# Kernel optimization log

Measured on AMD Instinct MI355X. Metric: run time of the kernel, lower is better.

Reference implementation:

```python
import jax, jax.numpy as jnp
import numpy as np

# hyperparameters (see init_kwargs)
DP, DS, DO, D, K, C = 256, 256, 64, 320, 10, 10
SI, NS = 100, 22
ALIGN = 0.05
COEF = 0.3989422917366028  # 1/sqrt(2*pi)
B, SEQ, T_STEPS = 32, 512, 200


def _linear_params(key, fan_in, fan_out):
    # torch nn.Linear default init: U(-1/sqrt(fan_in), 1/sqrt(fan_in))
    s = 1.0 / np.sqrt(fan_in)
    kw, kb = jax.random.split(key)
    w = jax.random.uniform(kw, (fan_in, fan_out), minval=-s, maxval=s, dtype=jnp.float32)
    b = jax.random.uniform(kb, (fan_out,), minval=-s, maxval=s, dtype=jnp.float32)
    return w, b


def setup_inputs() -> dict:
    key = jax.random.key(0)
    ks = jax.random.split(key, 8)
    sentence = jax.random.randint(ks[0], (B, SEQ), 0, SI)
    speaker_id = jax.random.randint(ks[1], (B,), 0, NS)
    Lut_P = jax.random.normal(ks[2], (SI, DP), dtype=jnp.float32)
    Lut_S = jax.random.normal(ks[3], (NS, DS), dtype=jnp.float32)
    Na_w, Na_b = _linear_params(ks[4], D * K, 3 * C)
    Nu_w, Nu_b = _linear_params(ks[5], D * K, D)
    No_w, No_b = _linear_params(ks[6], D * K, DO)
    kf = jax.random.split(ks[7], 2)
    Fu_w, Fu_b = _linear_params(kf[0], DS, DP)
    Fo_w, Fo_b = _linear_params(kf[1], DS, D * K)
    return dict(sentence=sentence, speaker_id=speaker_id, Lut_P=Lut_P, Lut_S=Lut_S,
                Na_w=Na_w, Na_b=Na_b, Nu_w=Nu_w, Nu_b=Nu_b, No_w=No_w, No_b=No_b,
                Fu_w=Fu_w, Fu_b=Fu_b, Fo_w=Fo_w, Fo_b=Fo_b, T=T_STEPS)


def reference(sentence, speaker_id, Lut_P, Lut_S, Na_w, Na_b, Nu_w, Nu_b,
              No_w, No_b, Fu_w, Fu_b, Fo_w, Fo_b, T):
    batch, seq_len = sentence.shape
    # Encoder: embedding lookups
    lut_p = Lut_P[sentence]          # (B, S, dp)
    ident = Lut_S[speaker_id]        # (B, ds)

    # ident-dependent terms are loop-invariant; hoist out of the scan
    idt = jnp.tanh(ident @ Fu_w + Fu_b)   # (B, dp)
    fo = ident @ Fo_w + Fo_b              # (B, d*k)

    # initialize(): buffer seeded with speaker embedding in first dp rows
    S0 = jnp.zeros((batch, D, K), dtype=lut_p.dtype)
    S0 = S0.at[:, :DP, :].set(ident[:, :, None])
    mu0 = jnp.zeros((batch, C), dtype=lut_p.dtype)
    o0 = jnp.zeros((batch, DO), dtype=lut_p.dtype)

    J = jnp.arange(1, seq_len + 1, dtype=lut_p.dtype)  # (S,)

    def step(carry, _):
        S_tm1, mu_tm1, o_tm1 = carry
        # --- GMM attention ---
        out = (S_tm1.reshape(batch, D * K) @ Na_w + Na_b).reshape(batch, 3, C)
        k_t, b_t, y_t = out[:, 0], out[:, 1], out[:, 2]
        mu_t = mu_tm1 + ALIGN * jnp.exp(k_t)            # (B, c)
        sig_t = jnp.exp(b_t)                            # (B, c)
        g_t = jax.nn.softmax(y_t, axis=1)               # (B, c)
        # phi: (B, c, S)
        phi = g_t[:, :, None] * jnp.exp(-0.5 * sig_t[:, :, None] * (mu_t[:, :, None] - J) ** 2)
        alpha = COEF * phi.sum(axis=1)                  # (B, S)
        c_t = jnp.einsum('bs,bsd->bd', alpha, lut_p)    # (B, dp)
        # --- Decoder buffer update ---
        C_t = jnp.concatenate([c_t + idt, o_tm1 / 30.0], axis=1)        # (B, d)
        Sp = jnp.concatenate([C_t[:, :, None], S_tm1[:, :, :-1]], axis=2)  # (B, d, k)
        u = Sp.reshape(batch, D * K) @ Nu_w + Nu_b                      # (B, d)
        S_t = jnp.concatenate([u[:, :, None], S_tm1[:, :, :-1]], axis=2)
        o_t = (S_t.reshape(batch, D * K) + fo) @ No_w + No_b            # (B, do)
        return (S_t, mu_t, o_t), o_t

    (_, _, _), outs = jax.lax.scan(step, (S0, mu0, o0), None, length=T)
    return outs  # (T, B, do)
```

## Files before the change

kernel.cpp:

```cpp
#include <hip/hip_runtime.h>

#define DP   256
#define DD   320
#define KK   10
#define CC   10
#define DOUT 64
#define SEQn 512
#define BB   32
#define SI   100
#define NSL  32
#define NGR  8
#define BPG  4
#define NTH  640
#define DPS  10
#define RPS  100

#define CFBASE 1024
#define PSA   448
#define UF_O  0
#define ZA_O  40
#define ZO_O  168
#define HALF_A (NGR*NSL*PSA)
#define PSB   320
#define PUBA_OFF 2048
#define PUBB_OFF (PUBA_OFF + 2*HALF_A)

typedef float f4 __attribute__((ext_vector_type(4)));

__device__ __forceinline__ void llc_ld(f4* dst, const float* p) {
    f4 r;
    asm volatile("global_load_dwordx4 %0, %1, off sc0 sc1" : "=&v"(r) : "v"(p));
    asm volatile("s_waitcnt vmcnt(0)" ::: "memory");
    __builtin_amdgcn_sched_barrier(0);
    *dst = r;
}
__device__ __forceinline__ void llc_st(float* p, f4 v) {
    asm volatile("global_store_dwordx4 %0, %1, off sc0 sc1" :: "v"(p), "v"(v) : "memory");
}

__global__ void prep_kernel(int* ctr) {
    int i = blockIdx.x * blockDim.x + threadIdx.x;
    if (i < 2048) ctr[i] = 0;
}

__device__ __forceinline__ void gbar8(int* base, int slice, int target) {
    asm volatile("s_waitcnt vmcnt(0)" ::: "memory");
    __syncthreads();
    if (threadIdx.x == 0)
        __hip_atomic_fetch_add(&base[(slice & 7) * 16], 1, __ATOMIC_RELEASE, __HIP_MEMORY_SCOPE_AGENT);
    if (threadIdx.x < 8) {
        for (;;) {
            int v = __hip_atomic_load(&base[threadIdx.x * 16], __ATOMIC_RELAXED, __HIP_MEMORY_SCOPE_AGENT);
            v += __shfl_xor(v, 1, 8);
            v += __shfl_xor(v, 2, 8);
            v += __shfl_xor(v, 4, 8);
            if (v >= target) break;
            __builtin_amdgcn_s_sleep(2);
        }
    }
    __syncthreads();
}

__global__ __launch_bounds__(NTH) void recur_kernel(
    const int* __restrict__ sentence, const int* __restrict__ speaker,
    const float* __restrict__ LutP, const float* __restrict__ LutS,
    const float* __restrict__ NaW,  const float* __restrict__ NaB,
    const float* __restrict__ NuW,  const float* __restrict__ NuB,
    const float* __restrict__ NoW,  const float* __restrict__ NoB,
    const float* __restrict__ FuW,  const float* __restrict__ FuB,
    const float* __restrict__ FoW,  const float* __restrict__ FoB,
    float* __restrict__ ws, const int* __restrict__ Tptr,
    float* __restrict__ out)
{
    const int tid  = threadIdx.x;
    const int s    = blockIdx.x & (NSL - 1);
    const int g    = blockIdx.x >> 5;
    const bool owner = (s < BPG);
    const int dbase = s * DPS;
    const int rbase = s * RPS;
    int*  ctr  = (int*)ws + g * 128;
    int*  CFg  = (int*)ws + CFBASE + g * 64;
    float* pubA = ws + PUBA_OFF;
    float* pubB = ws + PUBB_OFF;

    const int c_   = tid >> 6;
    const int lane = tid & 63;

    __shared__ float xsE[BPG][3328];
    __shared__ float wNa[RPS][32];
    __shared__ float wNo[RPS][65];
    __shared__ float naT0[DPS][32];
    __shared__ float noT0[DPS][65];
    __shared__ float identsh[BPG][DP];
    __shared__ float ufull[BPG][DD];
    __shared__ float colL[BPG][DD];
    __shared__ float ucol[BPG*DPS];
    __shared__ float zr[BPG*32];
    __shared__ float zor[BPG*DOUT];
    __shared__ float zastage[NSL][32];
    __shared__ float zostage[NSL][DOUT];
    __shared__ float fos[BPG][RPS];
    __shared__ float nubO[DPS];
    __shared__ float nabL[32];
    __shared__ float aoutL[32];
    __shared__ float muL[CC], sgL[CC], ggL[CC];
    __shared__ float alphaL[SEQn];
    __shared__ float histL[SI];
    __shared__ float idtF[DP];
    __shared__ float colF[DD];
    __shared__ float o_own[DOUT];
    __shared__ float foNoL[DOUT];
    __shared__ int   sentL[SEQn];
    __shared__ int   posidx[SEQn];
    __shared__ int   vstart[SI + 1];
    __shared__ int   vcnt[SI];

    for (int i = tid; i < RPS * 30; i += NTH) {
        int r = i / 30, c = i % 30;
        wNa[r][c] = NaW[(rbase + r) * 30 + c];
    }
    for (int i = tid; i < RPS * 64; i += NTH) {
        int r = i / 64, o = i % 64;
        wNo[r][o] = NoW[(rbase + r) * 64 + o];
    }
    if (tid < DPS * 30) { int dl = tid / 30, c = tid % 30; naT0[dl][c] = NaW[((dbase + dl) * KK) * 30 + c]; }
    if (tid < DPS * 64) { int dl = tid >> 6, o = tid & 63; noT0[dl][o] = NoW[((dbase + dl) * KK) * 64 + o]; }
    if (tid < DPS) nubO[tid] = NuB[dbase + tid];
    if (tid >= 16 && tid < 48) { int c = tid - 16; nabL[c] = (c < 30) ? NaB[c] : 0.f; }
    for (int i = tid; i < BPG * DP; i += NTH) {
        int j = i / DP, v = i % DP;
        identsh[j][v] = LutS[speaker[g * BPG + j] * DP + v];
    }
    __syncthreads();

    float w[50];
    #pragma unroll
    for (int q = 0; q < 50; ++q)
        w[q] = NuW[(size_t)(lane * 50 + q) * DD + dbase + c_];

    for (int i = tid; i < BPG * RPS; i += NTH) {
        int j = i / RPS, r = i % RPS;
        float acc = FoB[rbase + r];
        for (int v = 0; v < DP; v += 8) {
            float wv[8];
            #pragma unroll
            for (int e = 0; e < 8; ++e) wv[e] = FoW[(v + e) * 3200 + rbase + r];
            #pragma unroll
            for (int e = 0; e < 8; ++e) acc += identsh[j][v + e] * wv[e];
        }
        fos[j][r] = acc;
    }
    if (owner) {
        if (tid < DP) {
            float acc = FuB[tid];
            for (int v = 0; v < DP; v += 8) {
                float wv[8];
                #pragma unroll
                for (int e = 0; e < 8; ++e) wv[e] = FuW[(v + e) * DP + tid];
                #pragma unroll
                for (int e = 0; e < 8; ++e) acc += identsh[s][v + e] * wv[e];
            }
            idtF[tid] = tanhf(acc);
        }
        if (tid >= 512 && tid < 512 + CC) muL[tid - 512] = 0.f;
        if (tid < SEQn) sentL[tid] = sentence[(g * BPG + s) * SEQn + tid];
        __syncthreads();
        if (tid < SI) { int cnt = 0; for (int q = 0; q < SEQn; ++q) if (sentL[q] == tid) ++cnt; vcnt[tid] = cnt; }
        __syncthreads();
        if (tid == 0) { int run = 0; for (int v = 0; v < SI; ++v) { vstart[v] = run; run += vcnt[v]; } vstart[SI] = run; }
        __syncthreads();
        if (tid < SI) { int k = vstart[tid]; for (int q = 0; q < SEQn; ++q) if (sentL[q] == tid) posidx[k++] = q; }
    }
    for (int i = tid; i < BPG * 3200; i += NTH) {
        int j = i / 3200, row = i % 3200;
        int d = row / KK;
        xsE[j][(row / 50) * 52 + (row % 50)] = (d < DP) ? identsh[j][d] : 0.f;
    }
    __syncthreads();
    if (tid < 128) {
        int j = tid >> 5, c = tid & 31;
        float acc = 0.f;
        if (c < 30)
            for (int rr = 0; rr < RPS; ++rr) {
                int row = rbase + rr;
                acc += xsE[j][(row / 50) * 52 + (row % 50)] * wNa[rr][c];
            }
        zr[j * 32 + c] = acc;
    }
    if (tid >= 128 && tid < 384) {
        int t = tid - 128, j = t >> 6, o = t & 63;
        float acc = 0.f;
        for (int rr = 0; rr < RPS; ++rr) acc += fos[j][rr] * wNo[rr][o];
        zor[j * 64 + o] = acc;
    }
    __syncthreads();
    {
        float* pa0 = pubA + (size_t)(g * NSL + s) * PSA;
        if (tid < 32) llc_st(pa0 + ZA_O + tid * 4, *(f4*)&zr[tid * 4]);
        if (tid >= 32 && tid < 96) { int q = tid - 32; llc_st(pa0 + ZO_O + q * 4, *(f4*)&zor[q * 4]); }
    }
    gbar8(ctr, s, 32 * 1);

    const int T = Tptr[0];

    for (int i = 0; i < T; ++i) {
        const int rh = i & 1, wh = rh ^ 1;
        float* pa_r = pubA + (size_t)rh * HALF_A + (size_t)g * NSL * PSA;
        float* pa_w = pubA + (size_t)wh * HALF_A + (size_t)(g * NSL + s) * PSA;

        if (i > 0 && tid < 320) {
            int p = tid / 10, q = tid % 10;
            f4 v; llc_ld(&v, pa_r + p * PSA + UF_O + q * 4);
            #pragma unroll
            for (int e = 0; e < 4; ++e) {
                int f = q * 4 + e;
                ufull[f / 10][p * 10 + (f % 10)] = v[e];
            }
        }
        __syncthreads();

        if (owner) {
            f4 v_za = {0.f,0.f,0.f,0.f}, v_zo = {0.f,0.f,0.f,0.f};
            if (tid < 256) {
                const float* p = pa_r + (tid >> 3) * PSA + ZA_O + s * 32 + (tid & 7) * 4;
                asm volatile("global_load_dwordx4 %0, %1, off sc0 sc1" : "=&v"(v_za) : "v"(p));
            }
            if (tid < 512) {
                const float* p = pa_r + (tid >> 4) * PSA + ZO_O + s * 64 + (tid & 15) * 4;
                asm volatile("global_load_dwordx4 %0, %1, off sc0 sc1" : "=&v"(v_zo) : "v"(p));
            }
            asm volatile("s_waitcnt vmcnt(0)" ::: "memory");
            __builtin_amdgcn_sched_barrier(0);
            if (tid < 256) *(f4*)&zastage[tid >> 3][(tid & 7) * 4] = v_za;
            if (tid < 512) *(f4*)&zostage[tid >> 4][(tid & 15) * 4] = v_zo;
            __syncthreads();
            if (tid < 30) {
                float a = nabL[tid];
                for (int p = 0; p < NSL; ++p) a += zastage[p][tid];
                aoutL[tid] = a;
            }
            if (tid >= 64 && tid < 128) {
                int o = tid - 64;
                float v = 0.f;
                for (int p = 0; p < NSL; ++p) v += zostage[p][o];
                if (i == 0) { foNoL[o] = NoB[o] + v; o_own[o] = 0.f; }
                else        o_own[o] = foNoL[o] + v;
            }
            __syncthreads();
            if (tid < CC) {
                muL[tid] += 0.05f * expf(aoutL[tid]);
                sgL[tid] = expf(aoutL[10 + tid]);
                float m = -1e30f;
                for (int q = 0; q < CC; ++q) m = fmaxf(m, aoutL[20 + q]);
                float ssum = 0.f;
                for (int q = 0; q < CC; ++q) ssum += expf(aoutL[20 + q] - m);
                ggL[tid] = expf(aoutL[20 + tid] - m) / ssum;
            }
            __syncthreads();
            if (tid < SEQn) {
                float J = (float)(tid + 1);
                float a = 0.f;
                #pragma unroll
                for (int c = 0; c < CC; ++c) { float dm = muL[c] - J; a += ggL[c] * __expf(-0.5f * sgL[c] * dm * dm); }
                alphaL[tid] = a * 0.3989422917366028f;
            }
            __syncthreads();
            if (tid < SI) {
                float h = 0.f;
                for (int k = vstart[tid]; k < vstart[tid + 1]; ++k) h += alphaL[posidx[k]];
                histL[tid] = h;
            }
            __syncthreads();
            if (tid < DP) {
                float acc = idtF[tid];
                for (int v = 0; v < SI; v += 10) {
                    float wv[10];
                    #pragma unroll
                    for (int e = 0; e < 10; ++e) wv[e] = LutP[(v + e) * DP + tid];
                    #pragma unroll
                    for (int e = 0; e < 10; ++e) acc += histL[v + e] * wv[e];
                }
                colF[tid] = acc;
            } else if (tid < DD) {
                colF[tid] = o_own[tid - DP] * (1.0f / 30.0f);
            }
            __syncthreads();
            if (i > 0 && tid < DOUT)
                out[((size_t)(i - 1) * BB + (g * BPG + s)) * DOUT + tid] = o_own[tid];
            if (tid < 80) llc_st(pubB + (size_t)(g * BPG + s) * PSB + tid * 4, *(f4*)&colF[tid * 4]);
            asm volatile("s_waitcnt vmcnt(0)" ::: "memory");
            __syncthreads();
            if (tid == 0)
                __hip_atomic_store(&CFg[s * 16], i + 1, __ATOMIC_RELEASE, __HIP_MEMORY_SCOPE_AGENT);
        }

        for (int it = tid; it < BPG * DD; it += NTH) {
            int j = it / DD, d = it % DD;
            float* p = &xsE[j][(d / 5) * 52 + (d % 5) * 10];
            float t0 = p[0];
            float v1 = p[1], v2 = p[2], v3 = p[3], v4 = p[4], v5 = p[5], v6 = p[6], v7 = p[7], v8 = p[8];
            p[1] = (i == 0) ? t0 : ufull[j][d];
            p[2] = v1; p[3] = v2; p[4] = v3; p[5] = v4; p[6] = v5; p[7] = v6; p[8] = v7; p[9] = v8;
        }
        if (tid < BPG) {
            while (__hip_atomic_load(&CFg[tid * 16], __ATOMIC_RELAXED, __HIP_MEMORY_SCOPE_AGENT) < i + 1)
                __builtin_amdgcn_s_sleep(2);
        }
        __syncthreads();

        if (tid < 320) {
            int j = tid / 80, q = tid % 80;
            f4 v; llc_ld(&v, pubB + (size_t)(g * BPG + j) * PSB + q * 4);
            #pragma unroll
            for (int e = 0; e < 4; ++e) colL[j][q * 4 + e] = v[e];
        }
        __syncthreads();
        for (int it = tid; it < BPG * DD; it += NTH) {
            int j = it / DD, d = it % DD;
            xsE[j][(d / 5) * 52 + (d % 5) * 10] = colL[j][d];
        }
        __syncthreads();

        {
            float accE[BPG];
            #pragma unroll
            for (int j = 0; j < BPG; ++j) {
                const float* xb = &xsE[j][lane * 52];
                float a = 0.f;
                #pragma unroll
                for (int qq = 0; qq < 12; ++qq) {
                    f4 x = *(const f4*)(xb + qq * 4);
                    a += x.x * w[qq * 4] + x.y * w[qq * 4 + 1] + x.z * w[qq * 4 + 2] + x.w * w[qq * 4 + 3];
                }
                a += xb[48] * w[48] + xb[49] * w[49];
                accE[j] = a;
            }
            #pragma unroll
            for (int j = 0; j < BPG; ++j)
                for (int off = 32; off; off >>= 1) accE[j] += __shfl_xor(accE[j], off, 64);
            if (lane == 0) {
                #pragma unroll
                for (int j = 0; j < BPG; ++j) ucol[j * DPS + c_] = accE[j] + nubO[c_];
            }
        }
        __syncthreads();

        if (tid < 128) {
            int j = tid >> 5, c = tid & 31;
            float acc = 0.f;
            if (c < 30) {
                for (int dd = 0; dd < DPS; ++dd) {
                    int rg = 2 * s + (dd >= 5);
                    int of = dd * 10 - (dd >= 5 ? 50 : 0);
                    const float* xb = &xsE[j][rg * 52 + of];
                    #pragma unroll
                    for (int k = 1; k < KK; ++k) acc += xb[k] * wNa[dd * 10 + k][c];
                }
                #pragma unroll
                for (int dl = 0; dl < DPS; ++dl) acc += ucol[j * DPS + dl] * naT0[dl][c];
            }
            zr[j * 32 + c] = acc;
        }
        if (tid >= 128 && tid < 384) {
            int t = tid - 128, j = t >> 6, o = t & 63;
            float acc = 0.f;
            for (int dd = 0; dd < DPS; ++dd) {
                int rg = 2 * s + (dd >= 5);
                int of = dd * 10 - (dd >= 5 ? 50 : 0);
                const float* xb = &xsE[j][rg * 52 + of];
                #pragma unroll
                for (int k = 1; k < KK; ++k) acc += xb[k] * wNo[dd * 10 + k][o];
            }
            #pragma unroll
            for (int dl = 0; dl < DPS; ++dl) acc += ucol[j * DPS + dl] * noT0[dl][o];
            zor[j * 64 + o] = acc;
        }
        __syncthreads();

        if (tid < 10)                llc_st(pa_w + UF_O + tid * 4,        *(f4*)&ucol[tid * 4]);
        if (tid >= 10 && tid < 42)  { int q = tid - 10; llc_st(pa_w + ZA_O + q * 4, *(f4*)&zr[q * 4]); }
        if (tid >= 42 && tid < 106) { int q = tid - 42; llc_st(pa_w + ZO_O + q * 4, *(f4*)&zor[q * 4]); }
        gbar8(ctr, s, 32 * (i + 2));
    }

    if (owner) {
        const float* pa_r = pubA + (size_t)(T & 1) * HALF_A + (size_t)g * NSL * PSA;
        if (tid < 512) {
            f4 v; llc_ld(&v, pa_r + (tid >> 4) * PSA + ZO_O + s * 64 + (tid & 15) * 4);
            *(f4*)&zostage[tid >> 4][(tid & 15) * 4] = v;
        }
        __syncthreads();
        if (tid < DOUT) {
            float v = foNoL[tid];
            for (int p = 0; p < NSL; ++p) v += zostage[p][tid];
            out[((size_t)(T - 1) * BB + (g * BPG + s)) * DOUT + tid] = v;
        }
    }
}

extern "C" void kernel_launch(void* const* d_in, const int* in_sizes, int n_in,
                              void* d_out, int out_size, void* d_ws, size_t ws_size,
                              hipStream_t stream) {
    const int*   sentence = (const int*)d_in[0];
    const int*   speaker  = (const int*)d_in[1];
    const float* LutP = (const float*)d_in[2];
    const float* LutS = (const float*)d_in[3];
    const float* NaW  = (const float*)d_in[4];
    const float* NaB  = (const float*)d_in[5];
    const float* NuW  = (const float*)d_in[6];
    const float* NuB  = (const float*)d_in[7];
    const float* NoW  = (const float*)d_in[8];
    const float* NoB  = (const float*)d_in[9];
    const float* FuW  = (const float*)d_in[10];
    const float* FuB  = (const float*)d_in[11];
    const float* FoW  = (const float*)d_in[12];
    const float* FoB  = (const float*)d_in[13];
    const int*   Tptr = (const int*)d_in[14];
    float* ws   = (float*)d_ws;
    float* outp = (float*)d_out;

    hipLaunchKernelGGL(prep_kernel, dim3(2), dim3(1024), 0, stream, (int*)d_ws);
    hipLaunchKernelGGL(recur_kernel, dim3(NSL * NGR), dim3(NTH), 0, stream,
                       sentence, speaker, LutP, LutS, NaW, NaB,
                       NuW, NuB, NoW, NoB, FuW, FuB, FoW, FoB,
                       ws, Tptr, outp);
}
```

Baseline: 4.701 ms.

## Compute attention redundantly in every block to drop owner-to-slice handoff

Every block in a group now computes the attention, histogram and context column for all four batch rows itself, where before the four owner blocks did this and published the result through a separate buffer with a per-step flag spin-wait. This removes one cross-block synchronisation and a global round-trip per step. The partial sums are also stored transposed (slice-major per output element), so each reader reduces 32 contiguous values with wide loads instead of staging and summing in shared memory. The cost is four times the attention work in every block, serialised over the batch rows, plus more shared memory and scalar stores.

```diff
diff --git a/kernel.cpp b/kernel.cpp
--- a/kernel.cpp
+++ b/kernel.cpp
@@ -15,15 +15,9 @@
 #define DPS  10
 #define RPS  100
 
-#define CFBASE 1024
-#define PSA   448
-#define UF_O  0
-#define ZA_O  40
-#define ZO_O  168
-#define HALF_A (NGR*NSL*PSA)
-#define PSB   320
+#define GSZ   13568
+#define HALF  (NGR*GSZ)
 #define PUBA_OFF 2048
-#define PUBB_OFF (PUBA_OFF + 2*HALF_A)
 
 typedef float f4 __attribute__((ext_vector_type(4)));
 
@@ -36,6 +30,9 @@
 }
 __device__ __forceinline__ void llc_st(float* p, f4 v) {
     asm volatile("global_store_dwordx4 %0, %1, off sc0 sc1" :: "v"(p), "v"(v) : "memory");
+}
+__device__ __forceinline__ void llc_st1(float* p, float v) {
+    asm volatile("global_store_dword %0, %1, off sc0 sc1" :: "v"(p), "v"(v) : "memory");
 }
 
 __global__ void prep_kernel(int* ctr) {
@@ -75,13 +72,10 @@
     const int tid  = threadIdx.x;
     const int s    = blockIdx.x & (NSL - 1);
     const int g    = blockIdx.x >> 5;
-    const bool owner = (s < BPG);
     const int dbase = s * DPS;
     const int rbase = s * RPS;
     int*  ctr  = (int*)ws + g * 128;
-    int*  CFg  = (int*)ws + CFBASE + g * 64;
     float* pubA = ws + PUBA_OFF;
-    float* pubB = ws + PUBB_OFF;
 
     const int c_   = tid >> 6;
     const int lane = tid & 63;
@@ -91,29 +85,27 @@
     __shared__ float wNo[RPS][65];
     __shared__ float naT0[DPS][32];
     __shared__ float noT0[DPS][65];
-    __shared__ float identsh[BPG][DP];
     __shared__ float ufull[BPG][DD];
     __shared__ float colL[BPG][DD];
     __shared__ float ucol[BPG*DPS];
     __shared__ float zr[BPG*32];
     __shared__ float zor[BPG*DOUT];
-    __shared__ float zastage[NSL][32];
-    __shared__ float zostage[NSL][DOUT];
+    __shared__ float aout4[BPG][32];
+    __shared__ float oprev4[BPG][DOUT];
+    __shared__ float foNo4[BPG][DOUT];
+    __shared__ float mu4[BPG][CC], sg4[BPG][CC], gg4[BPG][CC];
+    __shared__ float alphaL[SEQn];
+    __shared__ float hist4[BPG][104];
+    __shared__ float idtF4[BPG][DP];
+    __shared__ float identsh[BPG][DP];
     __shared__ float fos[BPG][RPS];
     __shared__ float nubO[DPS];
     __shared__ float nabL[32];
-    __shared__ float aoutL[32];
-    __shared__ float muL[CC], sgL[CC], ggL[CC];
-    __shared__ float alphaL[SEQn];
-    __shared__ float histL[SI];
-    __shared__ float idtF[DP];
-    __shared__ float colF[DD];
-    __shared__ float o_own[DOUT];
-    __shared__ float foNoL[DOUT];
-    __shared__ int   sentL[SEQn];
-    __shared__ int   posidx[SEQn];
-    __shared__ int   vstart[SI + 1];
-    __shared__ int   vcnt[SI];
+    __shared__ float zred[DOUT][9];
+    __shared__ int   sentL4[BPG][SEQn];
+    __shared__ short posidx4[BPG][SEQn];
+    __shared__ int   vstart4[BPG][104];
+    __shared__ int   vcnt[104];
 
     for (int i = tid; i < RPS * 30; i += NTH) {
         int r = i / 30, c = i % 30;
@@ -127,10 +119,13 @@
     if (tid < DPS * 64) { int dl = tid >> 6, o = tid & 63; noT0[dl][o] = NoW[((dbase + dl) * KK) * 64 + o]; }
     if (tid < DPS) nubO[tid] = NuB[dbase + tid];
     if (tid >= 16 && tid < 48) { int c = tid - 16; nabL[c] = (c < 30) ? NaB[c] : 0.f; }
+    if (tid >= 64 && tid < 104) mu4[(tid - 64) / 10][(tid - 64) % 10] = 0.f;
     for (int i = tid; i < BPG * DP; i += NTH) {
         int j = i / DP, v = i % DP;
         identsh[j][v] = LutS[speaker[g * BPG + j] * DP + v];
     }
+    for (int i = tid; i < BPG * SEQn; i += NTH)
+        sentL4[i / SEQn][i % SEQn] = sentence[(g * BPG + i / SEQn) * SEQn + i % SEQn];
     __syncthreads();
 
     float w[50];
@@ -150,26 +145,26 @@
         }
         fos[j][r] = acc;
     }
-    if (owner) {
-        if (tid < DP) {
-            float acc = FuB[tid];
-            for (int v = 0; v < DP; v += 8) {
-                float wv[8];
-                #pragma unroll
-                for (int e = 0; e < 8; ++e) wv[e] = FuW[(v + e) * DP + tid];
-                #pragma unroll
-                for (int e = 0; e < 8; ++e) acc += identsh[s][v + e] * wv[e];
-            }
-            idtF[tid] = tanhf(acc);
-        }
-        if (tid >= 512 && tid < 512 + CC) muL[tid - 512] = 0.f;
-        if (tid < SEQn) sentL[tid] = sentence[(g * BPG + s) * SEQn + tid];
-        __syncthreads();
-        if (tid < SI) { int cnt = 0; for (int q = 0; q < SEQn; ++q) if (sentL[q] == tid) ++cnt; vcnt[tid] = cnt; }
-        __syncthreads();
-        if (tid == 0) { int run = 0; for (int v = 0; v < SI; ++v) { vstart[v] = run; run += vcnt[v]; } vstart[SI] = run; }
-        __syncthreads();
-        if (tid < SI) { int k = vstart[tid]; for (int q = 0; q < SEQn; ++q) if (sentL[q] == tid) posidx[k++] = q; }
+    for (int idx = tid; idx < BPG * DP; idx += NTH) {
+        int j = idx / DP, d = idx % DP;
+        float acc = FuB[d];
+        for (int v = 0; v < DP; v += 8) {
+            float wv[8];
+            #pragma unroll
+            for (int e = 0; e < 8; ++e) wv[e] = FuW[(v + e) * DP + d];
+            #pragma unroll
+            for (int e = 0; e < 8; ++e) acc += identsh[j][v + e] * wv[e];
+        }
+        idtF4[j][d] = tanhf(acc);
+    }
+    __syncthreads();
+    for (int j = 0; j < BPG; ++j) {
+        if (tid < SI) { int cnt = 0; for (int q = 0; q < SEQn; ++q) cnt += (sentL4[j][q] == tid); vcnt[tid] = cnt; }
+        __syncthreads();
+        if (tid == 0) { int run = 0; for (int v = 0; v < SI; ++v) { vstart4[j][v] = run; run += vcnt[v]; } vstart4[j][SI] = run; }
+        __syncthreads();
+        if (tid < SI) { int k = vstart4[j][tid]; for (int q = 0; q < SEQn; ++q) if (sentL4[j][q] == tid) posidx4[j][k++] = (short)q; }
+        __syncthreads();
     }
     for (int i = tid; i < BPG * 3200; i += NTH) {
         int j = i / 3200, row = i % 3200;
@@ -195,9 +190,9 @@
     }
     __syncthreads();
     {
-        float* pa0 = pubA + (size_t)(g * NSL + s) * PSA;
-        if (tid < 32) llc_st(pa0 + ZA_O + tid * 4, *(f4*)&zr[tid * 4]);
-        if (tid >= 32 && tid < 96) { int q = tid - 32; llc_st(pa0 + ZO_O + q * 4, *(f4*)&zor[q * 4]); }
+        float* pz = pubA + (size_t)g * GSZ + 1280;
+        if (tid < 128) { int j = tid >> 5, c = tid & 31; if (c < 30) llc_st1(pz + ((j * 96 + c) << 5) + s, zr[j * 32 + c]); }
+        if (tid >= 128 && tid < 384) { int t = tid - 128; int j = t >> 6, o = t & 63; llc_st1(pz + ((j * 96 + 32 + o) << 5) + s, zor[j * 64 + o]); }
     }
     gbar8(ctr, s, 32 * 1);
 
@@ -205,119 +200,127 @@
 
     for (int i = 0; i < T; ++i) {
         const int rh = i & 1, wh = rh ^ 1;
-        float* pa_r = pubA + (size_t)rh * HALF_A + (size_t)g * NSL * PSA;
-        float* pa_w = pubA + (size_t)wh * HALF_A + (size_t)(g * NSL + s) * PSA;
-
-        if (i > 0 && tid < 320) {
-            int p = tid / 10, q = tid % 10;
-            f4 v; llc_ld(&v, pa_r + p * PSA + UF_O + q * 4);
-            #pragma unroll
-            for (int e = 0; e < 4; ++e) {
-                int f = q * 4 + e;
-                ufull[f / 10][p * 10 + (f % 10)] = v[e];
-            }
-        }
-        __syncthreads();
-
-        if (owner) {
-            f4 v_za = {0.f,0.f,0.f,0.f}, v_zo = {0.f,0.f,0.f,0.f};
-            if (tid < 256) {
-                const float* p = pa_r + (tid >> 3) * PSA + ZA_O + s * 32 + (tid & 7) * 4;
-                asm volatile("global_load_dwordx4 %0, %1, off sc0 sc1" : "=&v"(v_za) : "v"(p));
-            }
-            if (tid < 512) {
-                const float* p = pa_r + (tid >> 4) * PSA + ZO_O + s * 64 + (tid & 15) * 4;
-                asm volatile("global_load_dwordx4 %0, %1, off sc0 sc1" : "=&v"(v_zo) : "v"(p));
+        const float* pa_r = pubA + (size_t)rh * HALF + (size_t)g * GSZ;
+        float* pa_w = pubA + (size_t)wh * HALF + (size_t)g * GSZ;
+
+        {
+            f4 zv0,zv1,zv2,zv3,zv4,zv5,zv6,zv7;
+            f4 ufa = {0,0,0,0}, ufb = {0,0,0,0};
+            const bool hz = (tid < 384);
+            const int zj = tid / 96, zc = tid % 96;
+            if (hz) {
+                const float* base = pa_r + 1280 + ((zj * 96 + zc) << 5);
+                asm volatile("global_load_dwordx4 %0, %1, off sc0 sc1" : "=&v"(zv0) : "v"(base));
+                asm volatile("global_load_dwordx4 %0, %1, off sc0 sc1" : "=&v"(zv1) : "v"(base + 4));
+                asm volatile("global_load_dwordx4 %0, %1, off sc0 sc1" : "=&v"(zv2) : "v"(base + 8));
+                asm volatile("global_load_dwordx4 %0, %1, off sc0 sc1" : "=&v"(zv3) : "v"(base + 12));
+                asm volatile("global_load_dwordx4 %0, %1, off sc0 sc1" : "=&v"(zv4) : "v"(base + 16));
+                asm volatile("global_load_dwordx4 %0, %1, off sc0 sc1" : "=&v"(zv5) : "v"(base + 20));
+                asm volatile("global_load_dwordx4 %0, %1, off sc0 sc1" : "=&v"(zv6) : "v"(base + 24));
+                asm volatile("global_load_dwordx4 %0, %1, off sc0 sc1" : "=&v"(zv7) : "v"(base + 28));
+            }
+            const bool hu = (i > 0 && tid >= 384);
+            const int ui = tid - 384;
+            if (hu) {
+                asm volatile("global_load_dwordx4 %0, %1, off sc0 sc1" : "=&v"(ufa) : "v"(pa_r + ui * 4));
+                if (ui < 64)
+                    asm volatile("global_load_dwordx4 %0, %1, off sc0 sc1" : "=&v"(ufb) : "v"(pa_r + (ui + 256) * 4));
             }
             asm volatile("s_waitcnt vmcnt(0)" ::: "memory");
             __builtin_amdgcn_sched_barrier(0);
-            if (tid < 256) *(f4*)&zastage[tid >> 3][(tid & 7) * 4] = v_za;
-            if (tid < 512) *(f4*)&zostage[tid >> 4][(tid & 15) * 4] = v_zo;
-            __syncthreads();
-            if (tid < 30) {
-                float a = nabL[tid];
-                for (int p = 0; p < NSL; ++p) a += zastage[p][tid];
-                aoutL[tid] = a;
-            }
-            if (tid >= 64 && tid < 128) {
-                int o = tid - 64;
+            if (hz) {
                 float v = 0.f;
-                for (int p = 0; p < NSL; ++p) v += zostage[p][o];
-                if (i == 0) { foNoL[o] = NoB[o] + v; o_own[o] = 0.f; }
-                else        o_own[o] = foNoL[o] + v;
-            }
-            __syncthreads();
+                v += zv0.x; v += zv0.y; v += zv0.z; v += zv0.w;
+                v += zv1.x; v += zv1.y; v += zv1.z; v += zv1.w;
+                v += zv2.x; v += zv2.y; v += zv2.z; v += zv2.w;
+                v += zv3.x; v += zv3.y; v += zv3.z; v += zv3.w;
+                v += zv4.x; v += zv4.y; v += zv4.z; v += zv4.w;
+                v += zv5.x; v += zv5.y; v += zv5.z; v += zv5.w;
+                v += zv6.x; v += zv6.y; v += zv6.z; v += zv6.w;
+                v += zv7.x; v += zv7.y; v += zv7.z; v += zv7.w;
+                if (zc < 30) {
+                    aout4[zj][zc] = nabL[zc] + v;
+                } else if (zc >= 32) {
+                    int o = zc - 32;
+                    if (i == 0) { foNo4[zj][o] = NoB[o] + v; oprev4[zj][o] = 0.f; }
+                    else        oprev4[zj][o] = foNo4[zj][o] + v;
+                }
+            }
+            if (hu) {
+                #pragma unroll
+                for (int e = 0; e < 4; ++e) {
+                    int f = ui * 4 + e, p = f / 40, r = f % 40;
+                    ufull[r / 10][p * 10 + r % 10] = ufa[e];
+                }
+                if (ui < 64) {
+                    #pragma unroll
+                    for (int e = 0; e < 4; ++e) {
+                        int f = (ui + 256) * 4 + e, p = f / 40, r = f % 40;
+                        ufull[r / 10][p * 10 + r % 10] = ufb[e];
+                    }
+                }
+            }
+        }
+        __syncthreads();
+        if (i > 0 && s < BPG && tid < DOUT)
+            out[((size_t)(i - 1) * BB + (g * BPG + s)) * DOUT + tid] = oprev4[s][tid];
+
+        for (int j = 0; j < BPG; ++j) {
             if (tid < CC) {
-                muL[tid] += 0.05f * expf(aoutL[tid]);
-                sgL[tid] = expf(aoutL[10 + tid]);
+                mu4[j][tid] += 0.05f * expf(aout4[j][tid]);
+                sg4[j][tid] = expf(aout4[j][10 + tid]);
                 float m = -1e30f;
-                for (int q = 0; q < CC; ++q) m = fmaxf(m, aoutL[20 + q]);
-                float ssum = 0.f;
-                for (int q = 0; q < CC; ++q) ssum += expf(aoutL[20 + q] - m);
-                ggL[tid] = expf(aoutL[20 + tid] - m) / ssum;
+                for (int q = 0; q < CC; ++q) m = fmaxf(m, aout4[j][20 + q]);
+                float ss = 0.f;
+                for (int q = 0; q < CC; ++q) ss += expf(aout4[j][20 + q] - m);
+                gg4[j][tid] = expf(aout4[j][20 + tid] - m) / ss;
             }
             __syncthreads();
             if (tid < SEQn) {
                 float J = (float)(tid + 1);
                 float a = 0.f;
                 #pragma unroll
-                for (int c = 0; c < CC; ++c) { float dm = muL[c] - J; a += ggL[c] * __expf(-0.5f * sgL[c] * dm * dm); }
+                for (int c = 0; c < CC; ++c) { float dm = mu4[j][c] - J; a += gg4[j][c] * __expf(-0.5f * sg4[j][c] * dm * dm); }
                 alphaL[tid] = a * 0.3989422917366028f;
             }
             __syncthreads();
             if (tid < SI) {
                 float h = 0.f;
-                for (int k = vstart[tid]; k < vstart[tid + 1]; ++k) h += alphaL[posidx[k]];
-                histL[tid] = h;
+                for (int k = vstart4[j][tid]; k < vstart4[j][tid + 1]; ++k) h += alphaL[posidx4[j][k]];
+                hist4[j][tid] = h;
             }
             __syncthreads();
-            if (tid < DP) {
-                float acc = idtF[tid];
-                for (int v = 0; v < SI; v += 10) {
-                    float wv[10];
-                    #pragma unroll
-                    for (int e = 0; e < 10; ++e) wv[e] = LutP[(v + e) * DP + tid];
-                    #pragma unroll
-                    for (int e = 0; e < 10; ++e) acc += histL[v + e] * wv[e];
-                }
-                colF[tid] = acc;
-            } else if (tid < DD) {
-                colF[tid] = o_own[tid - DP] * (1.0f / 30.0f);
-            }
-            __syncthreads();
-            if (i > 0 && tid < DOUT)
-                out[((size_t)(i - 1) * BB + (g * BPG + s)) * DOUT + tid] = o_own[tid];
-            if (tid < 80) llc_st(pubB + (size_t)(g * BPG + s) * PSB + tid * 4, *(f4*)&colF[tid * 4]);
-            asm volatile("s_waitcnt vmcnt(0)" ::: "memory");
-            __syncthreads();
-            if (tid == 0)
-                __hip_atomic_store(&CFg[s * 16], i + 1, __ATOMIC_RELEASE, __HIP_MEMORY_SCOPE_AGENT);
-        }
+        }
+        if (tid < DP) {
+            float a0 = idtF4[0][tid], a1 = idtF4[1][tid], a2 = idtF4[2][tid], a3 = idtF4[3][tid];
+            for (int v = 0; v < SI; v += 10) {
+                float wv[10];
+                #pragma unroll
+                for (int e = 0; e < 10; ++e) wv[e] = LutP[(v + e) * DP + tid];
+                #pragma unroll
+                for (int e = 0; e < 10; ++e) {
+                    a0 += hist4[0][v + e] * wv[e];
+                    a1 += hist4[1][v + e] * wv[e];
+                    a2 += hist4[2][v + e] * wv[e];
+                    a3 += hist4[3][v + e] * wv[e];
+                }
+            }
+            colL[0][tid] = a0; colL[1][tid] = a1; colL[2][tid] = a2; colL[3][tid] = a3;
+        } else if (tid < DP + DOUT) {
+            int o = tid - DP;
+            #pragma unroll
+            for (int j = 0; j < BPG; ++j) colL[j][DP + o] = oprev4[j][o] * (1.0f / 30.0f);
+        }
+        __syncthreads();
 
         for (int it = tid; it < BPG * DD; it += NTH) {
             int j = it / DD, d = it % DD;
             float* p = &xsE[j][(d / 5) * 52 + (d % 5) * 10];
             float t0 = p[0];
             float v1 = p[1], v2 = p[2], v3 = p[3], v4 = p[4], v5 = p[5], v6 = p[6], v7 = p[7], v8 = p[8];
+            p[0] = colL[j][d];
             p[1] = (i == 0) ? t0 : ufull[j][d];
             p[2] = v1; p[3] = v2; p[4] = v3; p[5] = v4; p[6] = v5; p[7] = v6; p[8] = v7; p[9] = v8;
-        }
-        if (tid < BPG) {
-            while (__hip_atomic_load(&CFg[tid * 16], __ATOMIC_RELAXED, __HIP_MEMORY_SCOPE_AGENT) < i + 1)
-                __builtin_amdgcn_s_sleep(2);
-        }
-        __syncthreads();
-
-        if (tid < 320) {
-            int j = tid / 80, q = tid % 80;
-            f4 v; llc_ld(&v, pubB + (size_t)(g * BPG + j) * PSB + q * 4);
-            #pragma unroll
-            for (int e = 0; e < 4; ++e) colL[j][q * 4 + e] = v[e];
-        }
-        __syncthreads();
-        for (int it = tid; it < BPG * DD; it += NTH) {
-            int j = it / DD, d = it % DD;
-            xsE[j][(d / 5) * 52 + (d % 5) * 10] = colL[j][d];
         }
         __syncthreads();
 
@@ -377,22 +380,33 @@
         }
         __syncthreads();
 
-        if (tid < 10)                llc_st(pa_w + UF_O + tid * 4,        *(f4*)&ucol[tid * 4]);
-        if (tid >= 10 && tid < 42)  { int q = tid - 10; llc_st(pa_w + ZA_O + q * 4, *(f4*)&zr[q * 4]); }
-        if (tid >= 42 && tid < 106) { int q = tid - 42; llc_st(pa_w + ZO_O + q * 4, *(f4*)&zor[q * 4]); }
+        if (tid < 10) llc_st(pa_w + s * 40 + tid * 4, *(f4*)&ucol[tid * 4]);
+        {
+            float* pz = pa_w + 1280;
+            if (tid >= 64 && tid < 192) {
+                int t = tid - 64, j = t >> 5, c = t & 31;
+                if (c < 30) llc_st1(pz + ((j * 96 + c) << 5) + s, zr[j * 32 + c]);
+            }
+            if (tid >= 192 && tid < 448) {
+                int t = tid - 192, j = t >> 6, o = t & 63;
+                llc_st1(pz + ((j * 96 + 32 + o) << 5) + s, zor[j * 64 + o]);
+            }
+        }
         gbar8(ctr, s, 32 * (i + 2));
     }
 
-    if (owner) {
-        const float* pa_r = pubA + (size_t)(T & 1) * HALF_A + (size_t)g * NSL * PSA;
+    if (s < BPG) {
+        const float* pa_r = pubA + (size_t)(T & 1) * HALF + (size_t)g * GSZ;
         if (tid < 512) {
-            f4 v; llc_ld(&v, pa_r + (tid >> 4) * PSA + ZO_O + s * 64 + (tid & 15) * 4);
-            *(f4*)&zostage[tid >> 4][(tid & 15) * 4] = v;
+            int o = tid >> 3, q = tid & 7;
+            f4 v; llc_ld(&v, pa_r + 1280 + ((s * 96 + 32 + o) << 5) + q * 4);
+            zred[o][q] = ((v.x + v.y) + (v.z + v.w));
         }
         __syncthreads();
         if (tid < DOUT) {
-            float v = foNoL[tid];
-            for (int p = 0; p < NSL; ++p) v += zostage[p][tid];
+            float v = foNo4[s][tid];
+            #pragma unroll
+            for (int q = 0; q < 8; ++q) v += zred[tid][q];
             out[((size_t)(T - 1) * BB + (g * BPG + s)) * DOUT + tid] = v;
         }
     }
```

Result: slower. 9.892 ms (+110.4%).
